# Performance work log

Measured on AMD Instinct MI355X. Metric: run time of the kernel, lower is better.

## Reference

```python
import jax, jax.numpy as jnp
import numpy as np

DIM = 1024
HEADS = 8
DIM_HEAD = 64
HIDDEN = HEADS * DIM_HEAD  # 512
SCALE = DIM_HEAD ** -0.5
BATCH = 16384
EPS = 1e-12  # F.normalize eps


def setup_inputs() -> dict:
    key = jax.random.key(0)
    k0, k1, k2 = jax.random.split(key, 3)
    x = jax.random.normal(k0, (BATCH, DIM), dtype=jnp.float32)
    w_qkv = jax.random.normal(k1, (3 * HIDDEN, DIM), dtype=jnp.float32) * 0.02
    w_out = jax.random.normal(k2, (DIM, HIDDEN), dtype=jnp.float32) * 0.02
    b_out = jnp.zeros((DIM,), dtype=jnp.float32)
    g = jnp.ones((1, DIM), dtype=jnp.float32)
    return {"x": x, "w_qkv": w_qkv, "w_out": w_out, "b_out": b_out, "g": g}


def reference(x, w_qkv, w_out, b_out, g):
    b = x.shape[0]
    # Conv1d(kernel=1, no bias) on n=1 sequence == matmul with (3*hidden, dim) weight
    qkv = x @ w_qkv.T  # (b, 3*hidden)
    q, k, v = jnp.split(qkv, 3, axis=1)  # each (b, hidden)
    # rearrange 'b (h c) n -> b h c n' with n=1 -> (b, h, c)
    q = q.reshape(b, HEADS, DIM_HEAD)
    k = k.reshape(b, HEADS, DIM_HEAD)
    v = v.reshape(b, HEADS, DIM_HEAD)
    # q.softmax(dim=-2) is over the c axis
    q = jax.nn.softmax(q, axis=-1) * SCALE
    # k.softmax(dim=-1) is over the n axis of size 1 -> all ones (kept faithful)
    k = jax.nn.softmax(k[..., None], axis=-1)[..., 0]
    # context = einsum('bhdn,bhen->bhde', k, v); out = einsum('bhde,bhdn->bhen', context, q)
    # with n=1 this collapses to out_e = (sum_d k_d q_d) * v_e; fused to avoid (b,h,d,e)
    s = jnp.einsum('bhd,bhd->bh', k, q)  # (b, h)
    out = s[..., None] * v  # (b, h, e)
    out = out.reshape(b, HIDDEN)  # 'b h c n -> b (h c) n', squeeze(-1)
    # Linear(hidden, dim)
    out = out @ w_out.T + b_out  # (b, dim)
    # RMSNorm_MLP: F.normalize(x, dim=1) * g * sqrt(dim)
    norm = jnp.linalg.norm(out, axis=1, keepdims=True)
    out = out / jnp.maximum(norm, EPS) * g * jnp.sqrt(jnp.float32(DIM))
    return out
```

## Files before the change

kernel.cpp:

```cpp
#include <hip/hip_runtime.h>
#include <hip/hip_bf16.h>


typedef __attribute__((ext_vector_type(8))) short bf16x8;
typedef __attribute__((ext_vector_type(4))) float f32x4;

struct alignas(16) bfvec8 { __hip_bfloat16 h[8]; };

__device__ __forceinline__ bfvec8 pack8(float4 a, float4 b) {
    bfvec8 o;
    o.h[0] = __float2bfloat16(a.x); o.h[1] = __float2bfloat16(a.y);
    o.h[2] = __float2bfloat16(a.z); o.h[3] = __float2bfloat16(a.w);
    o.h[4] = __float2bfloat16(b.x); o.h[5] = __float2bfloat16(b.y);
    o.h[6] = __float2bfloat16(b.z); o.h[7] = __float2bfloat16(b.w);
    return o;
}

__global__ __launch_bounds__(256)
void weff_fused(const float* __restrict__ Wo, const float* __restrict__ Wv,
                __hip_bfloat16* __restrict__ Weff) {
    __shared__ __align__(16) __hip_bfloat16 As[64 * 32];
    __shared__ __align__(16) __hip_bfloat16 Bs[64 * 32];
    __shared__ __align__(16) float Bf[32 * 65];

    const int tid  = threadIdx.x;
    const int lane = tid & 63;
    const int wave = tid >> 6;
    const int wm   = wave >> 1;
    const int wn   = wave & 1;
    const int quad = lane >> 4;
    const int tr   = lane & 15;
    const int m0   = blockIdx.y * 64;
    const int n0   = blockIdx.x * 64;

    f32x4 acc[2][2];
#pragma unroll
    for (int i = 0; i < 2; ++i)
#pragma unroll
        for (int j = 0; j < 2; ++j)
            acc[i][j] = (f32x4){0.f, 0.f, 0.f, 0.f};

    for (int kt = 0; kt < 512; kt += 32) {
        {
            int r = tid >> 2, c = tid & 3;
            int s = (r >> 1) & 3;
            int kg = (c ^ s) << 3;
            const float* sp = Wo + (size_t)(m0 + r) * 512 + kt + kg;
            float4 a = *(const float4*)sp, b = *(const float4*)(sp + 4);
            *(bfvec8*)(As + r * 32 + (c << 3)) = pack8(a, b);
        }
        {
            int kr = tid >> 3, c8 = (tid & 7) << 3;
            const float* sp = Wv + (size_t)(kt + kr) * 1024 + n0 + c8;
            float4 a = *(const float4*)sp, b = *(const float4*)(sp + 4);
            *(float4*)(Bf + kr * 65 + c8)     = a;
            *(float4*)(Bf + kr * 65 + c8 + 4) = b;
        }
        __syncthreads();
        {
            int n = tid >> 2, cc = tid & 3, k8 = cc << 3;
            float4 a, b;
            a.x = Bf[(k8 + 0) * 65 + n]; a.y = Bf[(k8 + 1) * 65 + n];
            a.z = Bf[(k8 + 2) * 65 + n]; a.w = Bf[(k8 + 3) * 65 + n];
            b.x = Bf[(k8 + 4) * 65 + n]; b.y = Bf[(k8 + 5) * 65 + n];
            b.z = Bf[(k8 + 6) * 65 + n]; b.w = Bf[(k8 + 7) * 65 + n];
            int cs = cc ^ ((n >> 1) & 3);
            *(bfvec8*)(Bs + n * 32 + cs * 8) = pack8(a, b);
        }
        __syncthreads();

        bf16x8 af[2], bf[2];
#pragma unroll
        for (int mi = 0; mi < 2; ++mi) {
            int r = wm * 32 + mi * 16 + tr;
            int c = quad ^ ((r >> 1) & 3);
            af[mi] = *(const bf16x8*)(As + r * 32 + c * 8);
        }
#pragma unroll
        for (int ni = 0; ni < 2; ++ni) {
            int r = wn * 32 + ni * 16 + tr;
            int c = quad ^ ((r >> 1) & 3);
            bf[ni] = *(const bf16x8*)(Bs + r * 32 + c * 8);
        }
#pragma unroll
        for (int mi = 0; mi < 2; ++mi)
#pragma unroll
            for (int ni = 0; ni < 2; ++ni)
                acc[mi][ni] = __builtin_amdgcn_mfma_f32_16x16x32_bf16(
                    af[mi], bf[ni], acc[mi][ni], 0, 0, 0);
        __syncthreads();
    }

#pragma unroll
    for (int mi = 0; mi < 2; ++mi)
#pragma unroll
        for (int ni = 0; ni < 2; ++ni) {
            const int col = n0 + wn * 32 + ni * 16 + tr;
#pragma unroll
            for (int r = 0; r < 4; ++r) {
                const int row = m0 + wm * 32 + mi * 16 + quad * 4 + r;
                Weff[(size_t)row * 1024 + col] =
                    __float2bfloat16(acc[mi][ni][r] * 0.125f);
            }
        }
}

__global__ __launch_bounds__(256)
void main_gemm(const float* __restrict__ X,
               const __hip_bfloat16* __restrict__ Bt,
               const float* __restrict__ bias,
               __hip_bfloat16* __restrict__ Y) {
    __shared__ __align__(16) __hip_bfloat16 As[128 * 64];
    __shared__ __align__(16) __hip_bfloat16 Bs[128 * 64];

    const int tid  = threadIdx.x;
    const int lane = tid & 63;
    const int wave = tid >> 6;
    const int wm   = wave >> 1;
    const int wn   = wave & 1;
    const int quad = lane >> 4;
    const int tr   = lane & 15;

    const int b   = blockIdx.x;
    const int xcd = b & 7;
    const int t   = b >> 3;
    const int nt  = t & 7;
    const int mt  = (t >> 3) * 8 + xcd;
    const int m0  = mt * 128;
    const int n0  = nt * 128;

    int rr[4], kgg[4];
    size_t abase[4];
#pragma unroll
    for (int i = 0; i < 4; ++i) {
        int L = i * 256 + tid;
        rr[i]  = L >> 3;
        int c  = L & 7;
        kgg[i] = (c ^ (rr[i] & 7)) << 3;
        abase[i] = (size_t)(m0 + rr[i]) * 1024 + kgg[i];
    }

    f32x4 acc[4][4];
#pragma unroll
    for (int i = 0; i < 4; ++i)
#pragma unroll
        for (int j = 0; j < 4; ++j)
            acc[i][j] = (f32x4){0.f, 0.f, 0.f, 0.f};

    float4 pa[4], pb[4];
#pragma unroll
    for (int i = 0; i < 4; ++i) {
        const float* s = X + abase[i];
        pa[i] = *(const float4*)s;
        pb[i] = *(const float4*)(s + 4);
    }

    for (int kt = 0; kt < 1024; kt += 64) {
#pragma unroll
        for (int i = 0; i < 4; ++i) {
            int L = i * 256 + tid;
            const __hip_bfloat16* gb = Bt + (size_t)(n0 + rr[i]) * 1024 + kt + kgg[i];
            __builtin_amdgcn_global_load_lds(
                (const __attribute__((address_space(1))) void*)gb,
                (__attribute__((address_space(3))) void*)(Bs + (size_t)L * 8), 16, 0, 0);
        }
#pragma unroll
        for (int i = 0; i < 4; ++i) {
            int L = i * 256 + tid;
            *(bfvec8*)(As + (size_t)L * 8) = pack8(pa[i], pb[i]);
        }
        __syncthreads();

        if (kt + 64 < 1024) {
#pragma unroll
            for (int i = 0; i < 4; ++i) {
                const float* s = X + abase[i] + kt + 64;
                pa[i] = *(const float4*)s;
                pb[i] = *(const float4*)(s + 4);
            }
        }

#pragma unroll
        for (int ko = 0; ko < 2; ++ko) {
            bf16x8 af[4], bf[4];
#pragma unroll
            for (int mi = 0; mi < 4; ++mi) {
                int r = wm * 64 + mi * 16 + tr;
                int c = (ko * 4 + quad) ^ (r & 7);
                af[mi] = *(const bf16x8*)(As + (r * 8 + c) * 8);
            }
#pragma unroll
            for (int ni = 0; ni < 4; ++ni) {
                int r = wn * 64 + ni * 16 + tr;
                int c = (ko * 4 + quad) ^ (r & 7);
                bf[ni] = *(const bf16x8*)(Bs + (r * 8 + c) * 8);
            }
#pragma unroll
            for (int mi = 0; mi < 4; ++mi)
#pragma unroll
                for (int ni = 0; ni < 4; ++ni)
                    acc[mi][ni] = __builtin_amdgcn_mfma_f32_16x16x32_bf16(
                        af[mi], bf[ni], acc[mi][ni], 0, 0, 0);
        }
        __syncthreads();
    }

#pragma unroll
    for (int mi = 0; mi < 4; ++mi)
#pragma unroll
        for (int ni = 0; ni < 4; ++ni) {
            const int col = n0 + wn * 64 + ni * 16 + tr;
            const float bv = bias[col];
#pragma unroll
            for (int r = 0; r < 4; ++r) {
                const int row = m0 + wm * 64 + mi * 16 + quad * 4 + r;
                Y[(size_t)row * 1024 + col] = __float2bfloat16(acc[mi][ni][r] + bv);
            }
        }
}

__global__ __launch_bounds__(256)
void rmsnorm2(const __hip_bfloat16* __restrict__ y, const float* __restrict__ g,
              float* __restrict__ out) {
    const int wave = threadIdx.x >> 6;
    const int sub  = wave >> 1;
    const int t    = threadIdx.x & 127;
    const int row  = blockIdx.x * 2 + sub;
    const size_t base = (size_t)row * 1024 + t * 8;

    union { uint4 u; ushort s[8]; } U;
    U.u = *(const uint4*)(y + base);
    float v[8];
#pragma unroll
    for (int j = 0; j < 8; ++j)
        v[j] = __bfloat162float(*(const __hip_bfloat16*)&U.s[j]);

    float ss = 0.f;
#pragma unroll
    for (int j = 0; j < 8; ++j) ss += v[j] * v[j];
#pragma unroll
    for (int off = 32; off > 0; off >>= 1)
        ss += __shfl_down(ss, off, 64);

    __shared__ float wsum[4];
    if ((threadIdx.x & 63) == 0) wsum[wave] = ss;
    __syncthreads();
    const float total = wsum[sub * 2] + wsum[sub * 2 + 1];
    const float sc = 32.0f / fmaxf(sqrtf(total), 1e-12f);

    const float4 g0 = *(const float4*)(g + t * 8);
    const float4 g1 = *(const float4*)(g + t * 8 + 4);
    float4 o0, o1;
    o0.x = v[0] * sc * g0.x; o0.y = v[1] * sc * g0.y;
    o0.z = v[2] * sc * g0.z; o0.w = v[3] * sc * g0.w;
    o1.x = v[4] * sc * g1.x; o1.y = v[5] * sc * g1.y;
    o1.z = v[6] * sc * g1.z; o1.w = v[7] * sc * g1.w;
    *(float4*)(out + base)     = o0;
    *(float4*)(out + base + 4) = o1;
}

extern "C" void kernel_launch(void* const* d_in, const int* in_sizes, int n_in,
                              void* d_out, int out_size, void* d_ws, size_t ws_size,
                              hipStream_t stream) {
    const float* x     = (const float*)d_in[0];
    const float* w_qkv = (const float*)d_in[1];
    const float* w_out = (const float*)d_in[2];
    const float* b_out = (const float*)d_in[3];
    const float* g     = (const float*)d_in[4];

    const int B = 16384, D = 1024, H = 512;
    const float* wv = w_qkv + (size_t)2 * H * D;

    char* ws = (char*)d_ws;
    size_t off = 0;
    __hip_bfloat16* weff_bf = (__hip_bfloat16*)(ws + off); off += (size_t)D * D * 2;
    __hip_bfloat16* y_bf    = (__hip_bfloat16*)(ws + off); off += (size_t)B * D * 2;

    weff_fused<<<dim3(D / 64, D / 64), 256, 0, stream>>>(w_out, wv, weff_bf);
    main_gemm<<<1024, 256, 0, stream>>>(x, weff_bf, b_out, y_bf);
    rmsnorm2<<<B / 2, 256, 0, stream>>>(y_bf, g, (float*)d_out);
}
```

Measured before the change: 193.0 us.

## Stage fp32 X tiles via direct global-to-LDS loads and coalesce output stores

The main GEMM now loads fp32 X tiles straight into LDS using global_load_lds with an XOR swizzle, and converts them to bf16 at fragment-read time. Previously they went through registers with a software prefetch and a pack-to-bf16 before the LDS store. The epilogue also stages the bf16 output tile in LDS, which is reused through a union, then writes full 16-byte rows to global memory instead of scattered 2-byte stores. The cost is double the LDS footprint for A, since it is held as fp32, plus repeated conversions per wave. The register prefetch that overlapped the next X load with compute is also gone.

After: 203.7 us. +5.6%, slower.

```diff
diff --git a/kernel.cpp b/kernel.cpp
--- a/kernel.cpp
+++ b/kernel.cpp
@@ -110,8 +110,10 @@
                const __hip_bfloat16* __restrict__ Bt,
                const float* __restrict__ bias,
                __hip_bfloat16* __restrict__ Y) {
-    __shared__ __align__(16) __hip_bfloat16 As[128 * 64];
-    __shared__ __align__(16) __hip_bfloat16 Bs[128 * 64];
+    __shared__ union __align__(16) {
+        struct { float Af[128 * 64]; ushort Bs[128 * 64]; } s;
+        ushort Ys[128 * 136];
+    } sh;
 
     const int tid  = threadIdx.x;
     const int lane = tid & 63;
@@ -129,15 +131,21 @@
     const int m0  = mt * 128;
     const int n0  = nt * 128;
 
-    int rr[4], kgg[4];
-    size_t abase[4];
+    int brr[4]; size_t bofs[4];
 #pragma unroll
     for (int i = 0; i < 4; ++i) {
         int L = i * 256 + tid;
-        rr[i]  = L >> 3;
+        brr[i] = L >> 3;
         int c  = L & 7;
-        kgg[i] = (c ^ (rr[i] & 7)) << 3;
-        abase[i] = (size_t)(m0 + rr[i]) * 1024 + kgg[i];
+        bofs[i] = (size_t)(n0 + brr[i]) * 1024 + ((c ^ (brr[i] & 7)) << 3);
+    }
+    size_t aofs[8];
+#pragma unroll
+    for (int i = 0; i < 8; ++i) {
+        int L = i * 256 + tid;
+        int r = L >> 4;
+        int c = L & 15;
+        aofs[i] = (size_t)(m0 + r) * 1024 + ((c ^ (r & 15)) << 2);
     }
 
     f32x4 acc[4][4];
@@ -147,53 +155,42 @@
         for (int j = 0; j < 4; ++j)
             acc[i][j] = (f32x4){0.f, 0.f, 0.f, 0.f};
 
-    float4 pa[4], pb[4];
-#pragma unroll
-    for (int i = 0; i < 4; ++i) {
-        const float* s = X + abase[i];
-        pa[i] = *(const float4*)s;
-        pb[i] = *(const float4*)(s + 4);
-    }
-
     for (int kt = 0; kt < 1024; kt += 64) {
+#pragma unroll
+        for (int i = 0; i < 8; ++i) {
+            int L = i * 256 + tid;
+            __builtin_amdgcn_global_load_lds(
+                (const __attribute__((address_space(1))) void*)(X + aofs[i] + kt),
+                (__attribute__((address_space(3))) void*)(sh.s.Af + (size_t)L * 4), 16, 0, 0);
+        }
 #pragma unroll
         for (int i = 0; i < 4; ++i) {
             int L = i * 256 + tid;
-            const __hip_bfloat16* gb = Bt + (size_t)(n0 + rr[i]) * 1024 + kt + kgg[i];
             __builtin_amdgcn_global_load_lds(
-                (const __attribute__((address_space(1))) void*)gb,
-                (__attribute__((address_space(3))) void*)(Bs + (size_t)L * 8), 16, 0, 0);
-        }
-#pragma unroll
-        for (int i = 0; i < 4; ++i) {
-            int L = i * 256 + tid;
-            *(bfvec8*)(As + (size_t)L * 8) = pack8(pa[i], pb[i]);
-        }
-        __syncthreads();
-
-        if (kt + 64 < 1024) {
-#pragma unroll
-            for (int i = 0; i < 4; ++i) {
-                const float* s = X + abase[i] + kt + 64;
-                pa[i] = *(const float4*)s;
-                pb[i] = *(const float4*)(s + 4);
-            }
-        }
+                (const __attribute__((address_space(1))) void*)(Bt + bofs[i] + kt),
+                (__attribute__((address_space(3))) void*)(sh.s.Bs + (size_t)L * 8), 16, 0, 0);
+        }
+        __syncthreads();
 
 #pragma unroll
         for (int ko = 0; ko < 2; ++ko) {
+            const int kb = ko * 8 + quad * 2;
             bf16x8 af[4], bf[4];
 #pragma unroll
             for (int mi = 0; mi < 4; ++mi) {
                 int r = wm * 64 + mi * 16 + tr;
-                int c = (ko * 4 + quad) ^ (r & 7);
-                af[mi] = *(const bf16x8*)(As + (r * 8 + c) * 8);
+                int sA = r & 15;
+                const float* base = sh.s.Af + r * 64;
+                float4 fa = *(const float4*)(base + ((kb ^ sA) << 2));
+                float4 fb = *(const float4*)(base + (((kb + 1) ^ sA) << 2));
+                bfvec8 u = pack8(fa, fb);
+                af[mi] = *(bf16x8*)&u;
             }
 #pragma unroll
             for (int ni = 0; ni < 4; ++ni) {
                 int r = wn * 64 + ni * 16 + tr;
                 int c = (ko * 4 + quad) ^ (r & 7);
-                bf[ni] = *(const bf16x8*)(Bs + (r * 8 + c) * 8);
+                bf[ni] = *(const bf16x8*)(sh.s.Bs + (r * 8 + c) * 8);
             }
 #pragma unroll
             for (int mi = 0; mi < 4; ++mi)
@@ -209,14 +206,28 @@
     for (int mi = 0; mi < 4; ++mi)
 #pragma unroll
         for (int ni = 0; ni < 4; ++ni) {
-            const int col = n0 + wn * 64 + ni * 16 + tr;
-            const float bv = bias[col];
+            const int cloc = wn * 64 + ni * 16 + tr;
+            const float bv = bias[n0 + cloc];
 #pragma unroll
             for (int r = 0; r < 4; ++r) {
-                const int row = m0 + wm * 64 + mi * 16 + quad * 4 + r;
-                Y[(size_t)row * 1024 + col] = __float2bfloat16(acc[mi][ni][r] + bv);
-            }
-        }
+                const int rloc = wm * 64 + mi * 16 + quad * 4 + r;
+                __hip_bfloat16 h = __float2bfloat16(acc[mi][ni][r] + bv);
+                sh.Ys[rloc * 136 + cloc] = *(ushort*)&h;
+            }
+        }
+    __syncthreads();
+
+    {
+        const int row  = tid >> 1;
+        const int half = tid & 1;
+        const ushort* src = sh.Ys + row * 136 + half * 64;
+        __hip_bfloat16* dst = Y + (size_t)(m0 + row) * 1024 + n0 + half * 64;
+#pragma unroll
+        for (int j = 0; j < 8; ++j) {
+            uint4 w = *(const uint4*)(src + j * 8);
+            *(uint4*)(dst + j * 8) = w;
+        }
+    }
 }
 
 __global__ __launch_bounds__(256)
```

## Pre-convert x to bf16 in prep kernel, fuse RMSNorm into GEMM via last-block counters

Applied to the files above, without the earlier changes.

Merges the W_eff product and a full fp32-to-bf16 conversion of x into one prep launch, so the GEMM can stream both operands straight to LDS with global_load_lds instead of converting in registers. The standalone RMSNorm kernel is replaced by a tail in the GEMM: per-row-tile atomic counters pick the last finishing N-tile block, which then normalizes the 128 rows from the bf16 Y buffer. This removes one launch and frees the GEMM's A path from conversion work. In exchange it adds an extra write and read of a bf16 copy of x, a memset, and a serialized normalization tail run by one block per row tile.

Result: slower. 325.5 us (+68.7%).

```diff
diff --git a/kernel.cpp b/kernel.cpp
--- a/kernel.cpp
+++ b/kernel.cpp
@@ -17,21 +17,30 @@
 }
 
 __global__ __launch_bounds__(256)
-void weff_fused(const float* __restrict__ Wo, const float* __restrict__ Wv,
-                __hip_bfloat16* __restrict__ Weff) {
+void prep(const float* __restrict__ Wo, const float* __restrict__ Wv,
+          __hip_bfloat16* __restrict__ Weff,
+          const float* __restrict__ x, bfvec8* __restrict__ x_bf) {
+    const int tid = threadIdx.x;
+
+    if (blockIdx.x >= 256) {
+        int i = (blockIdx.x - 256) * 256 + tid;
+        const float4* p = (const float4*)x + (size_t)i * 2;
+        x_bf[i] = pack8(p[0], p[1]);
+        return;
+    }
+
     __shared__ __align__(16) __hip_bfloat16 As[64 * 32];
     __shared__ __align__(16) __hip_bfloat16 Bs[64 * 32];
     __shared__ __align__(16) float Bf[32 * 65];
 
-    const int tid  = threadIdx.x;
     const int lane = tid & 63;
     const int wave = tid >> 6;
     const int wm   = wave >> 1;
     const int wn   = wave & 1;
     const int quad = lane >> 4;
     const int tr   = lane & 15;
-    const int m0   = blockIdx.y * 64;
-    const int n0   = blockIdx.x * 64;
+    const int m0   = (blockIdx.x >> 4) * 64;
+    const int n0   = (blockIdx.x & 15) * 64;
 
     f32x4 acc[2][2];
 #pragma unroll
@@ -106,10 +115,13 @@
 }
 
 __global__ __launch_bounds__(256)
-void main_gemm(const float* __restrict__ X,
+void gemm_norm(const __hip_bfloat16* __restrict__ A,
                const __hip_bfloat16* __restrict__ Bt,
                const float* __restrict__ bias,
-               __hip_bfloat16* __restrict__ Y) {
+               const float* __restrict__ g,
+               __hip_bfloat16* __restrict__ Y,
+               float* __restrict__ out,
+               unsigned int* __restrict__ counters) {
     __shared__ __align__(16) __hip_bfloat16 As[128 * 64];
     __shared__ __align__(16) __hip_bfloat16 Bs[128 * 64];
 
@@ -129,56 +141,36 @@
     const int m0  = mt * 128;
     const int n0  = nt * 128;
 
+    f32x4 acc[4][4];
+#pragma unroll
+    for (int i = 0; i < 4; ++i)
+#pragma unroll
+        for (int j = 0; j < 4; ++j)
+            acc[i][j] = (f32x4){0.f, 0.f, 0.f, 0.f};
+
     int rr[4], kgg[4];
-    size_t abase[4];
 #pragma unroll
     for (int i = 0; i < 4; ++i) {
         int L = i * 256 + tid;
         rr[i]  = L >> 3;
         int c  = L & 7;
         kgg[i] = (c ^ (rr[i] & 7)) << 3;
-        abase[i] = (size_t)(m0 + rr[i]) * 1024 + kgg[i];
-    }
-
-    f32x4 acc[4][4];
-#pragma unroll
-    for (int i = 0; i < 4; ++i)
-#pragma unroll
-        for (int j = 0; j < 4; ++j)
-            acc[i][j] = (f32x4){0.f, 0.f, 0.f, 0.f};
-
-    float4 pa[4], pb[4];
-#pragma unroll
-    for (int i = 0; i < 4; ++i) {
-        const float* s = X + abase[i];
-        pa[i] = *(const float4*)s;
-        pb[i] = *(const float4*)(s + 4);
     }
 
     for (int kt = 0; kt < 1024; kt += 64) {
 #pragma unroll
         for (int i = 0; i < 4; ++i) {
             int L = i * 256 + tid;
+            const __hip_bfloat16* ga = A  + (size_t)(m0 + rr[i]) * 1024 + kt + kgg[i];
             const __hip_bfloat16* gb = Bt + (size_t)(n0 + rr[i]) * 1024 + kt + kgg[i];
+            __builtin_amdgcn_global_load_lds(
+                (const __attribute__((address_space(1))) void*)ga,
+                (__attribute__((address_space(3))) void*)(As + (size_t)L * 8), 16, 0, 0);
             __builtin_amdgcn_global_load_lds(
                 (const __attribute__((address_space(1))) void*)gb,
                 (__attribute__((address_space(3))) void*)(Bs + (size_t)L * 8), 16, 0, 0);
         }
-#pragma unroll
-        for (int i = 0; i < 4; ++i) {
-            int L = i * 256 + tid;
-            *(bfvec8*)(As + (size_t)L * 8) = pack8(pa[i], pb[i]);
-        }
-        __syncthreads();
-
-        if (kt + 64 < 1024) {
-#pragma unroll
-            for (int i = 0; i < 4; ++i) {
-                const float* s = X + abase[i] + kt + 64;
-                pa[i] = *(const float4*)s;
-                pb[i] = *(const float4*)(s + 4);
-            }
-        }
+        __syncthreads();
 
 #pragma unroll
         for (int ko = 0; ko < 2; ++ko) {
@@ -217,46 +209,54 @@
                 Y[(size_t)row * 1024 + col] = __float2bfloat16(acc[mi][ni][r] + bv);
             }
         }
-}
-
-__global__ __launch_bounds__(256)
-void rmsnorm2(const __hip_bfloat16* __restrict__ y, const float* __restrict__ g,
-              float* __restrict__ out) {
-    const int wave = threadIdx.x >> 6;
-    const int sub  = wave >> 1;
-    const int t    = threadIdx.x & 127;
-    const int row  = blockIdx.x * 2 + sub;
-    const size_t base = (size_t)row * 1024 + t * 8;
-
-    union { uint4 u; ushort s[8]; } U;
-    U.u = *(const uint4*)(y + base);
-    float v[8];
-#pragma unroll
-    for (int j = 0; j < 8; ++j)
-        v[j] = __bfloat162float(*(const __hip_bfloat16*)&U.s[j]);
-
-    float ss = 0.f;
-#pragma unroll
-    for (int j = 0; j < 8; ++j) ss += v[j] * v[j];
-#pragma unroll
-    for (int off = 32; off > 0; off >>= 1)
-        ss += __shfl_down(ss, off, 64);
-
-    __shared__ float wsum[4];
-    if ((threadIdx.x & 63) == 0) wsum[wave] = ss;
+
     __syncthreads();
-    const float total = wsum[sub * 2] + wsum[sub * 2 + 1];
-    const float sc = 32.0f / fmaxf(sqrtf(total), 1e-12f);
-
-    const float4 g0 = *(const float4*)(g + t * 8);
-    const float4 g1 = *(const float4*)(g + t * 8 + 4);
-    float4 o0, o1;
-    o0.x = v[0] * sc * g0.x; o0.y = v[1] * sc * g0.y;
-    o0.z = v[2] * sc * g0.z; o0.w = v[3] * sc * g0.w;
-    o1.x = v[4] * sc * g1.x; o1.y = v[5] * sc * g1.y;
-    o1.z = v[6] * sc * g1.z; o1.w = v[7] * sc * g1.w;
-    *(float4*)(out + base)     = o0;
-    *(float4*)(out + base + 4) = o1;
+    __shared__ int is_last;
+    if (tid == 0) {
+        __threadfence();
+        unsigned int old = atomicAdd(&counters[mt], 1u);
+        is_last = (old == 7u);
+    }
+    __syncthreads();
+    if (!is_last) return;
+    __threadfence();
+
+    float4 g0 = *(const float4*)(g + lane * 16);
+    float4 g1 = *(const float4*)(g + lane * 16 + 4);
+    float4 g2 = *(const float4*)(g + lane * 16 + 8);
+    float4 g3 = *(const float4*)(g + lane * 16 + 12);
+
+    for (int it = 0; it < 32; ++it) {
+        const int row = m0 + it * 4 + wave;
+        const ushort* yp = (const ushort*)Y + (size_t)row * 1024 + lane * 16;
+        union { uint4 u; ushort s[8]; } U0, U1;
+        U0.u = *(const uint4*)yp;
+        U1.u = *(const uint4*)(yp + 8);
+        float v[16];
+#pragma unroll
+        for (int j = 0; j < 8; ++j) v[j]     = __bfloat162float(*(const __hip_bfloat16*)&U0.s[j]);
+#pragma unroll
+        for (int j = 0; j < 8; ++j) v[8 + j] = __bfloat162float(*(const __hip_bfloat16*)&U1.s[j]);
+
+        float ss = 0.f;
+#pragma unroll
+        for (int j = 0; j < 16; ++j) ss += v[j] * v[j];
+#pragma unroll
+        for (int off = 1; off < 64; off <<= 1)
+            ss += __shfl_xor(ss, off, 64);
+        const float sc = 32.0f / fmaxf(sqrtf(ss), 1e-12f);
+
+        float* op = out + (size_t)row * 1024 + lane * 16;
+        float4 o;
+        o.x = v[0]  * sc * g0.x; o.y = v[1]  * sc * g0.y; o.z = v[2]  * sc * g0.z; o.w = v[3]  * sc * g0.w;
+        *(float4*)(op)      = o;
+        o.x = v[4]  * sc * g1.x; o.y = v[5]  * sc * g1.y; o.z = v[6]  * sc * g1.z; o.w = v[7]  * sc * g1.w;
+        *(float4*)(op + 4)  = o;
+        o.x = v[8]  * sc * g2.x; o.y = v[9]  * sc * g2.y; o.z = v[10] * sc * g2.z; o.w = v[11] * sc * g2.w;
+        *(float4*)(op + 8)  = o;
+        o.x = v[12] * sc * g3.x; o.y = v[13] * sc * g3.y; o.z = v[14] * sc * g3.z; o.w = v[15] * sc * g3.w;
+        *(float4*)(op + 12) = o;
+    }
 }
 
 extern "C" void kernel_launch(void* const* d_in, const int* in_sizes, int n_in,
@@ -273,10 +273,12 @@
 
     char* ws = (char*)d_ws;
     size_t off = 0;
+    __hip_bfloat16* x_bf    = (__hip_bfloat16*)(ws + off); off += (size_t)B * D * 2;
     __hip_bfloat16* weff_bf = (__hip_bfloat16*)(ws + off); off += (size_t)D * D * 2;
     __hip_bfloat16* y_bf    = (__hip_bfloat16*)(ws + off); off += (size_t)B * D * 2;
-
-    weff_fused<<<dim3(D / 64, D / 64), 256, 0, stream>>>(w_out, wv, weff_bf);
-    main_gemm<<<1024, 256, 0, stream>>>(x, weff_bf, b_out, y_bf);
-    rmsnorm2<<<B / 2, 256, 0, stream>>>(y_bf, g, (float*)d_out);
-}
+    unsigned int*   counters = (unsigned int*)(ws + off);  off += 128 * sizeof(unsigned int);
+
+    hipMemsetAsync(counters, 0, 128 * sizeof(unsigned int), stream);
+    prep<<<256 + (B * D / 8) / 256, 256, 0, stream>>>(w_out, wv, weff_bf, x, (bfvec8*)x_bf);
+    gemm_norm<<<1024, 256, 0, stream>>>(x_bf, weff_bf, b_out, g, y_bf, (float*)d_out, counters);
+}
```
